# Kernel optimization log

Hardware: AMD Instinct MI355X
Metric: run time of the kernel (lower is better)

## Reference

```python
import jax, jax.numpy as jnp
import numpy as np

NEG_SLOPE = 0.2
EPS = 1e-16

N_NODES = 100000
N_EDGES = 1600000


def setup_inputs() -> dict:
    key = jax.random.key(0)
    ks = jax.random.split(key, 12)
    x = jax.random.normal(ks[0], (N_NODES, 4), dtype=jnp.float32)
    edge_index = jax.random.randint(ks[1], (2, N_EDGES), 0, N_NODES, dtype=jnp.int64)
    # conv1: GATConv(4, 32, heads=4)
    W1 = jax.random.normal(ks[2], (4, 4 * 32), dtype=jnp.float32) * (1.0 / np.sqrt(4))
    att_src1 = jax.random.normal(ks[3], (4, 32), dtype=jnp.float32) * 0.1
    att_dst1 = jax.random.normal(ks[4], (4, 32), dtype=jnp.float32) * 0.1
    b1 = jnp.zeros((4 * 32,), dtype=jnp.float32)
    # conv2: GATConv(128, 32, heads=1)
    W2 = jax.random.normal(ks[5], (128, 32), dtype=jnp.float32) * (1.0 / np.sqrt(128))
    att_src2 = jax.random.normal(ks[6], (1, 32), dtype=jnp.float32) * 0.1
    att_dst2 = jax.random.normal(ks[7], (1, 32), dtype=jnp.float32) * 0.1
    b2 = jnp.zeros((32,), dtype=jnp.float32)
    # lin: Linear(32, 2)
    lin_w = jax.random.normal(ks[8], (32, 2), dtype=jnp.float32) * (1.0 / np.sqrt(32))
    lin_b = jnp.zeros((2,), dtype=jnp.float32)
    return {"x": x, "edge_index": edge_index, "W1": W1, "att_src1": att_src1,
            "att_dst1": att_dst1, "b1": b1, "W2": W2, "att_src2": att_src2,
            "att_dst2": att_dst2, "b2": b2, "lin_w": lin_w, "lin_b": lin_b}


def gat_conv(x, src, dst, W, a_src, a_dst, bias, n_nodes):
    # x: [N, Fin]; W: [Fin, H*Fout]; a_src/a_dst: [H, Fout]
    H, Fout = a_src.shape
    xw = (x @ W).reshape(n_nodes, H, Fout)                      # [N, H, Fout]
    alpha_s = jnp.sum(xw * a_src[None], axis=-1)                # [N, H]
    alpha_d = jnp.sum(xw * a_dst[None], axis=-1)                # [N, H]
    e = alpha_s[src] + alpha_d[dst]                             # [E, H]
    e = jnp.where(e > 0, e, NEG_SLOPE * e)                      # leaky relu
    m = jax.ops.segment_max(e, dst, num_segments=n_nodes)      # softmax over incoming edges per target
    m = jnp.where(jnp.isfinite(m), m, 0.0)
    ex = jnp.exp(e - m[dst])
    s = jax.ops.segment_sum(ex, dst, num_segments=n_nodes)
    alpha = ex / (s[dst] + EPS)                                 # [E, H]
    msg = xw[src] * alpha[:, :, None]                           # [E, H, Fout]
    out = jax.ops.segment_sum(msg, dst, num_segments=n_nodes)  # [N, H, Fout]
    return out.reshape(n_nodes, H * Fout) + bias, alpha


def reference(x, edge_index, W1, att_src1, att_dst1, b1, W2, att_src2, att_dst2, b2, lin_w, lin_b):
    n = x.shape[0]
    # PyG GATConv default: add self loops
    loops = jnp.arange(n, dtype=edge_index.dtype)
    src = jnp.concatenate([edge_index[0], loops])
    dst = jnp.concatenate([edge_index[1], loops])
    h, _ = gat_conv(x, src, dst, W1, att_src1, att_dst1, b1, n)   # [N, 128]
    h = jax.nn.elu(h)
    h, attn = gat_conv(h, src, dst, W2, att_src2, att_dst2, b2, n)  # [N, 32], attn [E+N, 1]
    h = jax.nn.elu(h)
    pooled = jnp.mean(h, axis=0, keepdims=True)                   # [1, 32]
    logits = pooled @ lin_w + lin_b                               # [1, 2]
    return logits, attn
```

## Files before the change

### kernel.cpp

```cpp
#include <hip/hip_runtime.h>
#include <hip/hip_bf16.h>
#include <hip/hip_fp16.h>

#define NN 100000
#define NE 1600000
#define ET 1700000
#define NEG_SLOPE 0.2f
#define EPSI 1e-16f

#define SCAN_NB 98
#define DEG_PAD (SCAN_NB * 1024)

#define OFF_WF       0
#define OFF_AS1      32
#define OFF_AD1      400032
#define OFF_AS2      800032
#define OFF_AD2      900032
#define OFF_DEN2I    1000032
#define OFF_XW2H     1100032
#define OFF_MSG      1900032
#define OFF_OFFS     3500032
#define OFF_RANK     3600034
#define OFF_EDATA    5300034
#define OFF_POOLPART 7000036
#define OFF_DEG      7400036
#define OFF_POOL     7500388
#define OFF_BSUM     7500452
#define ZERO_START   OFF_DEG
#define ZERO_N4      ((DEG_PAD + 64) / 4)

__device__ __forceinline__ float lrelu(float v) { return v > 0.f ? v : NEG_SLOPE * v; }

__global__ void kz(float4* __restrict__ p, int n4) {
    int st = gridDim.x * 256;
    for (int i = blockIdx.x * 256 + threadIdx.x; i < n4; i += st)
        p[i] = make_float4(0.f, 0.f, 0.f, 0.f);
}

__global__ void k0_wfold(const float* __restrict__ W1, const float* __restrict__ aS1,
                         const float* __restrict__ aD1, float* __restrict__ wf) {
    int t = threadIdx.x;
    if (t < 32) {
        int u = t & 15, k = u >> 2, h = u & 3;
        const float* av = (t < 16) ? aS1 : aD1;
        float s = 0.f;
        for (int f = 0; f < 32; f++) s += W1[k * 128 + h * 32 + f] * av[h * 32 + f];
        wf[t] = s;
    }
}

__global__ void k1_att1(const float* __restrict__ x, const float* __restrict__ wf,
                        float* __restrict__ as1, float* __restrict__ ad1) {
    int n = blockIdx.x * 256 + threadIdx.x;
    if (n >= NN) return;
    float4 xv = *(const float4*)(x + n * 4);
#pragma unroll
    for (int h = 0; h < 4; h++) {
        as1[n * 4 + h] = xv.x * wf[h] + xv.y * wf[4 + h] + xv.z * wf[8 + h] + xv.w * wf[12 + h];
        ad1[n * 4 + h] = xv.x * wf[16 + h] + xv.y * wf[20 + h] + xv.z * wf[24 + h] + xv.w * wf[28 + h];
    }
}

__global__ void kc1_deg(const int* __restrict__ ei, int* __restrict__ deg,
                        int* __restrict__ rank) {
    int e = blockIdx.x * 256 + threadIdx.x;
    if (e >= ET) return;
    int d_ = (e < NE) ? ei[NE + e] : (e - NE);
    rank[e] = atomicAdd(&deg[d_], 1);
}

__global__ void kc2a(const int* __restrict__ deg, int* __restrict__ bsum) {
    __shared__ int ws_[4];
    int b = blockIdx.x, t = threadIdx.x;
    int4 d = *(const int4*)(deg + b * 1024 + t * 4);
    int s = d.x + d.y + d.z + d.w;
#pragma unroll
    for (int m = 1; m < 64; m <<= 1) s += __shfl_xor(s, m);
    if ((t & 63) == 0) ws_[t >> 6] = s;
    __syncthreads();
    if (t == 0) bsum[b] = ws_[0] + ws_[1] + ws_[2] + ws_[3];
}

__global__ void kc2c(const int* __restrict__ deg, const int* __restrict__ bsum,
                     int* __restrict__ offs) {
    __shared__ int bs[128];
    __shared__ int ts[256];
    int b = blockIdx.x, t = threadIdx.x;
    if (t < 128) bs[t] = (t < SCAN_NB) ? bsum[t] : 0;
    __syncthreads();
    for (int off = 1; off < 128; off <<= 1) {
        int u = (t >= off && t < 128) ? bs[t - off] : 0;
        __syncthreads();
        if (t < 128) bs[t] += u;
        __syncthreads();
    }
    int bpre = (b == 0) ? 0 : bs[b - 1];
    int base = b * 1024 + t * 4;
    int4 d = *(const int4*)(deg + base);
    int s = d.x + d.y + d.z + d.w;
    ts[t] = s;
    __syncthreads();
    for (int off = 1; off < 256; off <<= 1) {
        int u = (t >= off) ? ts[t - off] : 0;
        __syncthreads();
        ts[t] += u;
        __syncthreads();
    }
    int r = bpre + ((t == 0) ? 0 : ts[t - 1]);
    if (base < NN)     offs[base] = r;     r += d.x;
    if (base + 1 < NN) offs[base + 1] = r; r += d.y;
    if (base + 2 < NN) offs[base + 2] = r; r += d.z;
    if (base + 3 < NN) offs[base + 3] = r;
    if (b == 0 && t == 0) offs[NN] = bs[SCAN_NB - 1];
}

__global__ void kc3_fill(const int* __restrict__ ei, const int* __restrict__ offs,
                         const int* __restrict__ rank, int* __restrict__ edata) {
    int e = blockIdx.x * 256 + threadIdx.x;
    if (e >= ET) return;
    int s_, d_;
    if (e < NE) { s_ = ei[e]; d_ = ei[NE + e]; } else { s_ = d_ = e - NE; }
    edata[offs[d_] + rank[e]] = s_;
}

__global__ __launch_bounds__(256) void k4a_gather(
    const int* __restrict__ offs, const int* __restrict__ edata,
    const float* __restrict__ x, const float* __restrict__ as1,
    const float* __restrict__ ad1, float* __restrict__ msg) {
    int tid = threadIdx.x;
    int n = blockIdx.x * 16 + (tid >> 4);
    int q = tid & 15, h = q & 3, p = q >> 2;
    float ad = ad1[n * 4 + h];
    float z0 = 0.f, z1 = 0.f, z2 = 0.f, z3 = 0.f, den = 0.f;
    int beg = offs[n], end = offs[n + 1];
    for (int j = beg + p; j < end; j += 4) {
        int src = edata[j];
        float ex = __expf(lrelu(as1[src * 4 + h] + ad));
        float4 xv = *(const float4*)(x + src * 4);
        den += ex;
        z0 += ex * xv.x; z1 += ex * xv.y; z2 += ex * xv.z; z3 += ex * xv.w;
    }
#pragma unroll
    for (int m = 4; m <= 8; m <<= 1) {
        den += __shfl_xor(den, m);
        z0 += __shfl_xor(z0, m); z1 += __shfl_xor(z1, m);
        z2 += __shfl_xor(z2, m); z3 += __shfl_xor(z3, m);
    }
    if (p == 0) {
        float inv = 1.f / (den + EPSI);
        *(float4*)(msg + n * 16 + h * 4) = make_float4(z0 * inv, z1 * inv, z2 * inv, z3 * inv);
    }
}

__global__ __launch_bounds__(256) void k4b_dense(
    const float* __restrict__ msg, const float* __restrict__ W1,
    const float* __restrict__ b1, const float* __restrict__ W2,
    const float* __restrict__ aw_s2, const float* __restrict__ aw_d2,
    __half* __restrict__ xw2h, float* __restrict__ as2, float* __restrict__ ad2) {
    __shared__ float hs[4][128];
    int wv = threadIdx.x >> 6, ln = threadIdx.x & 63;
    int n = blockIdx.x * 4 + wv;
    int f0 = ln * 2;
    int h = f0 >> 5;
    float4 m = *(const float4*)(msg + n * 16 + h * 4);
    float h0 = m.x * W1[f0]     + m.y * W1[128 + f0]     + m.z * W1[256 + f0]     + m.w * W1[384 + f0]     + b1[f0];
    float h1 = m.x * W1[f0 + 1] + m.y * W1[128 + f0 + 1] + m.z * W1[256 + f0 + 1] + m.w * W1[384 + f0 + 1] + b1[f0 + 1];
    h0 = h0 > 0.f ? h0 : (__expf(h0) - 1.f);
    h1 = h1 > 0.f ? h1 : (__expf(h1) - 1.f);
    hs[wv][f0] = h0; hs[wv][f0 + 1] = h1;
    __syncthreads();
    int f = ln & 31, kb = (ln >> 5) * 64;
    float a = 0.f;
#pragma unroll
    for (int k = 0; k < 64; k++) a += hs[wv][kb + k] * W2[(kb + k) * 32 + f];
    a += __shfl_xor(a, 32);
    float ps = a * aw_s2[f], pd = a * aw_d2[f];
#pragma unroll
    for (int m2 = 1; m2 < 32; m2 <<= 1) { ps += __shfl_xor(ps, m2); pd += __shfl_xor(pd, m2); }
    if (ln < 32) xw2h[n * 32 + f] = __float2half_rn(a);
    if (ln == 0) { as2[n] = ps; ad2[n] = pd; }
}

__global__ __launch_bounds__(256) void k6_conv2(
    const int* __restrict__ offs, const int* __restrict__ edata,
    const __half* __restrict__ xw2h, const float* __restrict__ as2,
    const float* __restrict__ ad2, const float* __restrict__ b2,
    float* __restrict__ den2i, float* __restrict__ pool_part) {
    __shared__ float psum[4][32];
    int sub = threadIdx.x >> 5, f = threadIdx.x & 31;
    int n = blockIdx.x * 8 + sub;
    float ad = ad2[n];
    float den = 0.f, acc = 0.f;
    int beg = offs[n], end = offs[n + 1];
    for (int base = beg; base < end; base += 32) {
        int j = base + f;
        int src = 0;
        float ex = 0.f;
        if (j < end) {
            src = edata[j];
            ex = __expf(lrelu(as2[src] + ad));
        }
        den += ex;
        int cnt = min(32, end - base);
        for (int k = 0; k < cnt; k++) {
            int   sk = __shfl(src, k, 32);
            float ek = __shfl(ex, k, 32);
            acc += ek * __half2float(xw2h[sk * 32 + f]);
        }
    }
#pragma unroll
    for (int m = 1; m < 32; m <<= 1) den += __shfl_xor(den, m, 32);
    float inv = 1.f / (den + EPSI);
    if (f == 0) den2i[n] = inv;
    float v = acc * inv + b2[f];
    v = v > 0.f ? v : (__expf(v) - 1.f);
    v += __shfl_xor(v, 32);
    int wv = threadIdx.x >> 6;
    if ((threadIdx.x & 63) < 32) psum[wv][f] = v;
    __syncthreads();
    if (threadIdx.x < 32)
        pool_part[blockIdx.x * 32 + f] = psum[0][f] + psum[1][f] + psum[2][f] + psum[3][f];
}

__global__ void k7_attn(const int* __restrict__ ei, const float* __restrict__ as2,
                        const float* __restrict__ ad2, const float* __restrict__ den2i,
                        float* __restrict__ attn) {
    int e = blockIdx.x * 256 + threadIdx.x;
    if (e >= ET) return;
    int s_, d_;
    if (e < NE) { s_ = ei[e]; d_ = ei[NE + e]; } else { s_ = d_ = e - NE; }
    attn[e] = __expf(lrelu(as2[s_] + ad2[d_])) * den2i[d_];
}

__global__ void k8_pool(const float* __restrict__ pool_part, float* __restrict__ pool) {
    int tid = threadIdx.x;
    int f = tid & 31;
    float acc = 0.f;
    int st = gridDim.x * 256;
    for (int i = blockIdx.x * 256 + tid; i < 12500 * 32; i += st) acc += pool_part[i];
    acc += __shfl_xor(acc, 32);
    if ((tid & 63) < 32) unsafeAtomicAdd(&pool[f], acc);
}

__global__ void k9_logits(const float* __restrict__ pool, const float* __restrict__ lin_w,
                          const float* __restrict__ lin_b, float* __restrict__ out) {
    int j = threadIdx.x;
    if (j < 2) {
        float s = 0.f;
        for (int f = 0; f < 32; f++) s += (pool[f] * (1.0f / NN)) * lin_w[f * 2 + j];
        out[j] = s + lin_b[j];
    }
}

extern "C" void kernel_launch(void* const* d_in, const int* in_sizes, int n_in,
                              void* d_out, int out_size, void* d_ws, size_t ws_size,
                              hipStream_t stream) {
    const float* x    = (const float*)d_in[0];
    const int*   ei   = (const int*)d_in[1];
    const float* W1   = (const float*)d_in[2];
    const float* aS1  = (const float*)d_in[3];
    const float* aD1  = (const float*)d_in[4];
    const float* b1   = (const float*)d_in[5];
    const float* W2   = (const float*)d_in[6];
    const float* aS2  = (const float*)d_in[7];
    const float* aD2  = (const float*)d_in[8];
    const float* b2   = (const float*)d_in[9];
    const float* linw = (const float*)d_in[10];
    const float* linb = (const float*)d_in[11];

    float*  ws    = (float*)d_ws;
    float*  wf    = ws + OFF_WF;
    float*  as1   = ws + OFF_AS1;
    float*  ad1   = ws + OFF_AD1;
    float*  as2   = ws + OFF_AS2;
    float*  ad2   = ws + OFF_AD2;
    float*  den2i = ws + OFF_DEN2I;
    __half* xw2h  = (__half*)(ws + OFF_XW2H);
    float*  msg   = ws + OFF_MSG;
    int*    offs  = (int*)(ws + OFF_OFFS);
    int*    rank  = (int*)(ws + OFF_RANK);
    int*    ed    = (int*)(ws + OFF_EDATA);
    float*  ppart = ws + OFF_POOLPART;
    int*    deg   = (int*)(ws + OFF_DEG);
    float*  pool  = ws + OFF_POOL;
    int*    bsum  = (int*)(ws + OFF_BSUM);

    float* logits = (float*)d_out;
    float* attn   = (float*)d_out + 2;

    kz<<<98, 256, 0, stream>>>((float4*)(ws + ZERO_START), ZERO_N4);
    k0_wfold<<<1, 64, 0, stream>>>(W1, aS1, aD1, wf);
    k1_att1<<<(NN + 255) / 256, 256, 0, stream>>>(x, wf, as1, ad1);
    kc1_deg<<<(ET + 255) / 256, 256, 0, stream>>>(ei, deg, rank);
    kc2a<<<SCAN_NB, 256, 0, stream>>>(deg, bsum);
    kc2c<<<SCAN_NB, 256, 0, stream>>>(deg, bsum, offs);
    kc3_fill<<<(ET + 255) / 256, 256, 0, stream>>>(ei, offs, rank, ed);
    k4a_gather<<<NN / 16, 256, 0, stream>>>(offs, ed, x, as1, ad1, msg);
    k4b_dense<<<NN / 4, 256, 0, stream>>>(msg, W1, b1, W2, aS2, aD2, xw2h, as2, ad2);
    k6_conv2<<<NN / 8, 256, 0, stream>>>(offs, ed, xw2h, as2, ad2, b2, den2i, ppart);
    k7_attn<<<(ET + 255) / 256, 256, 0, stream>>>(ei, as2, ad2, den2i, attn);
    k8_pool<<<256, 256, 0, stream>>>(ppart, pool);
    k9_logits<<<1, 64, 0, stream>>>(pool, linw, linb, logits);
}
```

Baseline: 310.1 us.

## Fuse conv1 gather into dense conv2 projection kernel, one node per wavefront

Merges the conv1 attention-weighted gather and the dense W1/ELU/W2 projection into one kernel, with one 64-lane wavefront per node instead of 16 lanes per node. The 16-float per-node message now stays in registers and is broadcast by shuffle, so the global write and reread of msg and one kernel launch disappear. The W2 inner loop also reads the shared-memory row as float4. In exchange each node's edge gather uses 16 parallel strands, which may waste lanes on low-degree nodes, and the gather now runs at the dense stage's block granularity.

```diff
diff --git a/kernel.cpp b/kernel.cpp
--- a/kernel.cpp
+++ b/kernel.cpp
@@ -18,7 +18,6 @@
 #define OFF_AD2      900032
 #define OFF_DEN2I    1000032
 #define OFF_XW2H     1100032
-#define OFF_MSG      1900032
 #define OFF_OFFS     3500032
 #define OFF_RANK     3600034
 #define OFF_EDATA    5300034
@@ -123,56 +122,54 @@
     edata[offs[d_] + rank[e]] = s_;
 }
 
-__global__ __launch_bounds__(256) void k4a_gather(
+__global__ __launch_bounds__(256) void k4ab(
     const int* __restrict__ offs, const int* __restrict__ edata,
     const float* __restrict__ x, const float* __restrict__ as1,
-    const float* __restrict__ ad1, float* __restrict__ msg) {
-    int tid = threadIdx.x;
-    int n = blockIdx.x * 16 + (tid >> 4);
-    int q = tid & 15, h = q & 3, p = q >> 2;
-    float ad = ad1[n * 4 + h];
-    float z0 = 0.f, z1 = 0.f, z2 = 0.f, z3 = 0.f, den = 0.f;
-    int beg = offs[n], end = offs[n + 1];
-    for (int j = beg + p; j < end; j += 4) {
-        int src = edata[j];
-        float ex = __expf(lrelu(as1[src * 4 + h] + ad));
-        float4 xv = *(const float4*)(x + src * 4);
-        den += ex;
-        z0 += ex * xv.x; z1 += ex * xv.y; z2 += ex * xv.z; z3 += ex * xv.w;
-    }
-#pragma unroll
-    for (int m = 4; m <= 8; m <<= 1) {
-        den += __shfl_xor(den, m);
-        z0 += __shfl_xor(z0, m); z1 += __shfl_xor(z1, m);
-        z2 += __shfl_xor(z2, m); z3 += __shfl_xor(z3, m);
-    }
-    if (p == 0) {
-        float inv = 1.f / (den + EPSI);
-        *(float4*)(msg + n * 16 + h * 4) = make_float4(z0 * inv, z1 * inv, z2 * inv, z3 * inv);
-    }
-}
-
-__global__ __launch_bounds__(256) void k4b_dense(
-    const float* __restrict__ msg, const float* __restrict__ W1,
+    const float* __restrict__ ad1, const float* __restrict__ W1,
     const float* __restrict__ b1, const float* __restrict__ W2,
     const float* __restrict__ aw_s2, const float* __restrict__ aw_d2,
     __half* __restrict__ xw2h, float* __restrict__ as2, float* __restrict__ ad2) {
     __shared__ float hs[4][128];
     int wv = threadIdx.x >> 6, ln = threadIdx.x & 63;
     int n = blockIdx.x * 4 + wv;
-    int f0 = ln * 2;
-    int h = f0 >> 5;
-    float4 m = *(const float4*)(msg + n * 16 + h * 4);
-    float h0 = m.x * W1[f0]     + m.y * W1[128 + f0]     + m.z * W1[256 + f0]     + m.w * W1[384 + f0]     + b1[f0];
-    float h1 = m.x * W1[f0 + 1] + m.y * W1[128 + f0 + 1] + m.z * W1[256 + f0 + 1] + m.w * W1[384 + f0 + 1] + b1[f0 + 1];
+    int hq = ln & 3, p = ln >> 2;
+    float ad = ad1[n * 4 + hq];
+    float z0 = 0.f, z1 = 0.f, z2 = 0.f, z3 = 0.f, den = 0.f;
+    int beg = offs[n], end = offs[n + 1];
+    for (int j = beg + p; j < end; j += 16) {
+        int src = edata[j];
+        float ex = __expf(lrelu(as1[src * 4 + hq] + ad));
+        float4 xv = *(const float4*)(x + src * 4);
+        den += ex;
+        z0 += ex * xv.x; z1 += ex * xv.y; z2 += ex * xv.z; z3 += ex * xv.w;
+    }
+#pragma unroll
+    for (int m = 4; m <= 32; m <<= 1) {
+        den += __shfl_xor(den, m);
+        z0 += __shfl_xor(z0, m); z1 += __shfl_xor(z1, m);
+        z2 += __shfl_xor(z2, m); z3 += __shfl_xor(z3, m);
+    }
+    float inv = 1.f / (den + EPSI);
+    float v0 = z0 * inv, v1 = z1 * inv, v2 = z2 * inv, v3 = z3 * inv;
+    int f0 = ln * 2, h = ln >> 4;
+    float mx = __shfl(v0, h), my = __shfl(v1, h), mz = __shfl(v2, h), mw = __shfl(v3, h);
+    float h0 = mx * W1[f0]     + my * W1[128 + f0]     + mz * W1[256 + f0]     + mw * W1[384 + f0]     + b1[f0];
+    float h1 = mx * W1[f0 + 1] + my * W1[128 + f0 + 1] + mz * W1[256 + f0 + 1] + mw * W1[384 + f0 + 1] + b1[f0 + 1];
     h0 = h0 > 0.f ? h0 : (__expf(h0) - 1.f);
     h1 = h1 > 0.f ? h1 : (__expf(h1) - 1.f);
     hs[wv][f0] = h0; hs[wv][f0 + 1] = h1;
     __syncthreads();
     int f = ln & 31, kb = (ln >> 5) * 64;
+    const float* hrow = &hs[wv][kb];
     float a = 0.f;
 #pragma unroll
-    for (int k = 0; k < 64; k++) a += hs[wv][kb + k] * W2[(kb + k) * 32 + f];
+    for (int k = 0; k < 64; k += 4) {
+        float4 hv = *(const float4*)(hrow + k);
+        a += hv.x * W2[(kb + k) * 32 + f];
+        a += hv.y * W2[(kb + k + 1) * 32 + f];
+        a += hv.z * W2[(kb + k + 2) * 32 + f];
+        a += hv.w * W2[(kb + k + 3) * 32 + f];
+    }
     a += __shfl_xor(a, 32);
     float ps = a * aw_s2[f], pd = a * aw_d2[f];
 #pragma unroll
@@ -276,7 +273,6 @@
     float*  ad2   = ws + OFF_AD2;
     float*  den2i = ws + OFF_DEN2I;
     __half* xw2h  = (__half*)(ws + OFF_XW2H);
-    float*  msg   = ws + OFF_MSG;
     int*    offs  = (int*)(ws + OFF_OFFS);
     int*    rank  = (int*)(ws + OFF_RANK);
     int*    ed    = (int*)(ws + OFF_EDATA);
@@ -295,8 +291,8 @@
     kc2a<<<SCAN_NB, 256, 0, stream>>>(deg, bsum);
     kc2c<<<SCAN_NB, 256, 0, stream>>>(deg, bsum, offs);
     kc3_fill<<<(ET + 255) / 256, 256, 0, stream>>>(ei, offs, rank, ed);
-    k4a_gather<<<NN / 16, 256, 0, stream>>>(offs, ed, x, as1, ad1, msg);
-    k4b_dense<<<NN / 4, 256, 0, stream>>>(msg, W1, b1, W2, aS2, aD2, xw2h, as2, ad2);
+    k4ab<<<NN / 4, 256, 0, stream>>>(offs, ed, x, as1, ad1, W1, b1, W2,
+                                     aS2, aD2, xw2h, as2, ad2);
     k6_conv2<<<NN / 8, 256, 0, stream>>>(offs, ed, xw2h, as2, ad2, b2, den2i, ppart);
     k7_attn<<<(ET + 255) / 256, 256, 0, stream>>>(ei, as2, ad2, den2i, attn);
     k8_pool<<<256, 256, 0, stream>>>(ppart, pool);
```

Result: no change. 304.0 us (-2.0%).
